# Optimization experiments

Hardware: AMD Instinct MI355X
Metric: run time of the kernel (lower is better)

Reference implementation:

```python
import jax, jax.numpy as jnp
import numpy as np

K_LAYERS = 2   # top-k layers kept in zeta routing
K_EXPERTS = 2  # top-k experts kept in alpha routing


def _topk_sparse_softmax(logits, k):
    """Keep top-k along last axis, set rest to -inf, softmax. logits [..., N]."""
    lead = logits.shape[:-1]
    n = logits.shape[-1]
    flat = logits.reshape(-1, n)
    vals, idx = jax.lax.top_k(flat, k)                      # [R,k]
    sparse = jnp.full_like(flat, -jnp.inf)
    rows = jnp.arange(flat.shape[0])[:, None]
    sparse = sparse.at[rows, idx].set(vals)
    return jax.nn.softmax(sparse, axis=-1).reshape(*lead, n)


def _lora_layer(h, W, b, A, B, zeta_l, alpha_l):
    """One backbone Linear + gated LoRA expert mixture + ReLU.
    h [B,in], W [out,in], A [E,r,in], B [E,out,r], zeta_l [B], alpha_l [B,E].
    """
    lin = h @ W.T + b                                       # [B,out]
    t = jnp.einsum('bi,eri->ber', h, A)                     # [B,E,r]
    tw = t * alpha_l[:, :, None]                            # weight experts early
    lora_sum = jnp.einsum('ber,eor->bo', tw, B)             # [B,out]
    return jax.nn.relu(lin + zeta_l[:, None] * lora_sum)


def _routing(domain_ids, dom_emb, layer_pos, Wi1, bi1, Wi2, bi2,
             Wa1, ba1, Wa2, ba2, gate_logits, R_benefit):
    M, H = dom_emb.shape
    L = layer_pos.shape[0]
    router_inp = jnp.concatenate([
        jnp.broadcast_to(dom_emb[:, None, :], (M, L, H)),
        jnp.broadcast_to(layer_pos[None, :, :], (M, L, H)),
    ], axis=-1)                                             # [M,L,2H]
    hz = jax.nn.relu(router_inp @ Wi1.T + bi1)
    zeta_logits = (hz @ Wi2.T + bi2)[..., 0]                # [M,L]
    zeta_all = _topk_sparse_softmax(zeta_logits, K_LAYERS)
    ha = jax.nn.relu(router_inp @ Wa1.T + ba1)
    alpha_logits = ha @ Wa2.T + ba2                         # [M,L,E]
    alpha_all = _topk_sparse_softmax(alpha_logits, K_EXPERTS)
    # gated benefit matrix, row-normalized
    R = jax.nn.softplus(gate_logits) * R_benefit
    R = R / jnp.clip(R.sum(-1, keepdims=True), 1e-12)
    zeta_agg = R @ zeta_all                                 # [M,L]
    alpha_agg = jnp.einsum('mn,nle->mle', R, alpha_all)     # [M,L,E]
    return zeta_agg[domain_ids], alpha_agg[domain_ids]      # [B,L],[B,L,E]


def setup_inputs() -> dict:
    key = jax.random.key(0)
    ks = jax.random.split(key, 32)
    Bsz, D0, D1, D2, D3 = 16384, 2048, 2048, 1024, 512
    E, r, M, H, L = 4, 8, 8, 64, 3
    s = 0.02
    return {
        'x': jax.random.normal(ks[0], (Bsz, D0), jnp.float32),
        'domain_ids': jax.random.randint(ks[1], (Bsz,), 0, M),
        'W1': jax.random.normal(ks[2], (D1, D0)) * s, 'b1': jnp.zeros((D1,)),
        'W2': jax.random.normal(ks[3], (D2, D1)) * s, 'b2': jnp.zeros((D2,)),
        'W3': jax.random.normal(ks[4], (D3, D2)) * s, 'b3': jnp.zeros((D3,)),
        'A1': jax.random.normal(ks[5], (E, r, D0)) * s, 'B1': jax.random.normal(ks[6], (E, D1, r)) * s,
        'A2': jax.random.normal(ks[7], (E, r, D1)) * s, 'B2': jax.random.normal(ks[8], (E, D2, r)) * s,
        'A3': jax.random.normal(ks[9], (E, r, D2)) * s, 'B3': jax.random.normal(ks[10], (E, D3, r)) * s,
        'dom_emb': jax.random.normal(ks[11], (M, H)) * s,
        'layer_pos': jax.random.normal(ks[12], (L, H)) * s,
        'Wi1': jax.random.normal(ks[13], (H, 2 * H)) * 0.1, 'bi1': jnp.zeros((H,)),
        'Wi2': jax.random.normal(ks[14], (1, H)) * 0.1, 'bi2': jnp.zeros((1,)),
        'Wa1': jax.random.normal(ks[15], (H, 2 * H)) * 0.1, 'ba1': jnp.zeros((H,)),
        'Wa2': jax.random.normal(ks[16], (E, H)) * 0.1, 'ba2': jnp.zeros((E,)),
        'gate_logits': jax.random.normal(ks[17], (M, M)) * 0.1,
        'R_benefit': jax.random.uniform(ks[18], (M, M)),
    }


def reference(x, domain_ids, W1, b1, W2, b2, W3, b3,
              A1, B1, A2, B2, A3, B3,
              dom_emb, layer_pos, Wi1, bi1, Wi2, bi2,
              Wa1, ba1, Wa2, ba2, gate_logits, R_benefit):
    zeta, alpha = _routing(domain_ids, dom_emb, layer_pos, Wi1, bi1, Wi2, bi2,
                           Wa1, ba1, Wa2, ba2, gate_logits, R_benefit)
    h = _lora_layer(x, W1, b1, A1, B1, zeta[:, 0], alpha[:, 0])
    h = _lora_layer(h, W2, b2, A2, B2, zeta[:, 1], alpha[:, 1])
    h = _lora_layer(h, W3, b3, A3, B3, zeta[:, 2], alpha[:, 2])
    return h
```

## Files before the change

### kernel.cpp

```cpp
#include <hip/hip_runtime.h>

typedef __bf16 bf16_t;
typedef __bf16 bf16x8 __attribute__((ext_vector_type(8)));
typedef __bf16 bf16x4_v __attribute__((ext_vector_type(4)));
typedef float f32x4 __attribute__((ext_vector_type(4)));

#define AS1 __attribute__((address_space(1)))
#define AS3 __attribute__((address_space(3)))

__device__ __forceinline__ void gload_lds16(const void* g, void* l) {
    __builtin_amdgcn_global_load_lds((AS1 void*)(void*)g, (AS3 void*)l, 16, 0, 0);
}

__global__ void routing_kernel(
    const float* __restrict__ dom_emb, const float* __restrict__ layer_pos,
    const float* __restrict__ Wi1, const float* __restrict__ bi1,
    const float* __restrict__ Wi2, const float* __restrict__ bi2,
    const float* __restrict__ Wa1, const float* __restrict__ ba1,
    const float* __restrict__ Wa2, const float* __restrict__ ba2,
    const float* __restrict__ gate_logits, const float* __restrict__ R_benefit,
    float* __restrict__ salpha)
{
    constexpr int M = 8, L = 3, E = 4, H = 64;
    __shared__ float zl[M * L];
    __shared__ float al[M * L][E];
    __shared__ float zeta_all[M][L];
    __shared__ float alpha_all[M][L][E];
    const int t = threadIdx.x;
    const int ml = t >> 3, js = t & 7;
    if (ml < M * L) {
        const int m = ml / L, l = ml % L;
        float zacc = 0.f;
        float aacc[E] = {0.f, 0.f, 0.f, 0.f};
        for (int jj = 0; jj < 8; ++jj) {
            const int j = js * 8 + jj;
            float hz = bi1[j], ha = ba1[j];
            for (int i = 0; i < H; ++i) {
                const float de = dom_emb[m * H + i];
                const float lp = layer_pos[l * H + i];
                hz += de * Wi1[j * 2 * H + i] + lp * Wi1[j * 2 * H + H + i];
                ha += de * Wa1[j * 2 * H + i] + lp * Wa1[j * 2 * H + H + i];
            }
            hz = fmaxf(hz, 0.f); ha = fmaxf(ha, 0.f);
            zacc += hz * Wi2[j];
            for (int e = 0; e < E; ++e) aacc[e] += ha * Wa2[e * H + j];
        }
        #pragma unroll
        for (int off = 4; off >= 1; off >>= 1) {
            zacc += __shfl_down(zacc, off, 8);
            for (int e = 0; e < E; ++e) aacc[e] += __shfl_down(aacc[e], off, 8);
        }
        if (js == 0) {
            zl[ml] = zacc + bi2[0];
            for (int e = 0; e < E; ++e) al[ml][e] = aacc[e] + ba2[e];
        }
    }
    __syncthreads();
    if (t < M) {
        const int m = t;
        float v[3] = { zl[m * L + 0], zl[m * L + 1], zl[m * L + 2] };
        int di = 0; float dv = v[0];
        for (int i = 1; i < 3; ++i) if (v[i] <= dv) { dv = v[i]; di = i; }
        float mx = -1e30f;
        for (int i = 0; i < 3; ++i) if (i != di) mx = fmaxf(mx, v[i]);
        float s = 0.f, ev[3];
        for (int i = 0; i < 3; ++i) { ev[i] = (i == di) ? 0.f : expf(v[i] - mx); s += ev[i]; }
        for (int i = 0; i < 3; ++i) zeta_all[m][i] = ev[i] / s;
        for (int l = 0; l < L; ++l) {
            float a[4];
            for (int e = 0; e < 4; ++e) a[e] = al[m * L + l][e];
            int i1 = 0;
            for (int e = 1; e < 4; ++e) if (a[e] > a[i1]) i1 = e;
            int i2 = -1;
            for (int e = 0; e < 4; ++e) { if (e == i1) continue; if (i2 < 0 || a[e] > a[i2]) i2 = e; }
            const float mx2 = fmaxf(a[i1], a[i2]);
            const float e1 = expf(a[i1] - mx2), e2 = expf(a[i2] - mx2);
            const float ss = e1 + e2;
            for (int e = 0; e < 4; ++e) alpha_all[m][l][e] = 0.f;
            alpha_all[m][l][i1] = e1 / ss;
            alpha_all[m][l][i2] = e2 / ss;
        }
    }
    __syncthreads();
    if (t < M) {
        const int m = t;
        float Rrow[8]; float rs = 0.f;
        for (int n = 0; n < M; ++n) {
            const float g = gate_logits[m * M + n];
            const float rr = log1pf(expf(g)) * R_benefit[m * M + n];
            Rrow[n] = rr; rs += rr;
        }
        rs = fmaxf(rs, 1e-12f);
        for (int l = 0; l < L; ++l) {
            float zag = 0.f, aag[4] = {0.f, 0.f, 0.f, 0.f};
            for (int n = 0; n < M; ++n) {
                const float w = Rrow[n] / rs;
                zag += w * zeta_all[n][l];
                for (int e = 0; e < 4; ++e) aag[e] += w * alpha_all[n][l][e];
            }
            for (int e = 0; e < 4; ++e) salpha[(m * L + l) * 4 + e] = zag * aag[e];
        }
    }
}

__global__ void cvt_fused(const float* __restrict__ s0, const float* __restrict__ s1,
                          const float* __restrict__ s2, const float* __restrict__ s3,
                          const float* __restrict__ s4, const float* __restrict__ s5,
                          bf16_t* __restrict__ dst)
{
    const int i = blockIdx.x * 256 + threadIdx.x;
    constexpr int b0 = 1048576;
    constexpr int b1 = b0 + 524288;
    constexpr int b2 = b1 + 131072;
    constexpr int b3 = b2 + 16384;
    constexpr int b4 = b3 + 16384;
    constexpr int b5 = b4 + 8192;
    if (i >= b5) return;
    const float* src; int rel;
    if (i < b0)      { src = s0; rel = i; }
    else if (i < b1) { src = s1; rel = i - b0; }
    else if (i < b2) { src = s2; rel = i - b1; }
    else if (i < b3) { src = s3; rel = i - b2; }
    else if (i < b4) { src = s4; rel = i - b3; }
    else             { src = s5; rel = i - b4; }
    const float4 v = ((const float4*)src)[rel];
    bf16x4_v o;
    o[0] = (__bf16)v.x; o[1] = (__bf16)v.y; o[2] = (__bf16)v.z; o[3] = (__bf16)v.w;
    ((bf16x4_v*)dst)[i] = o;
}

__global__ void bepi_fused(const float* __restrict__ B1, const float* __restrict__ B2,
                           const float* __restrict__ B3, bf16_t* __restrict__ dst)
{
    const int idx = blockIdx.x * 256 + threadIdx.x;
    constexpr int c1 = 2048 * 32, c2 = c1 + 1024 * 32, c3 = c2 + 512 * 32;
    if (idx >= c3) return;
    const float* B; int rel, Dout;
    if (idx < c1)      { B = B1; rel = idx;      Dout = 2048; }
    else if (idx < c2) { B = B2; rel = idx - c1; Dout = 1024; }
    else               { B = B3; rel = idx - c2; Dout = 512; }
    const int o = rel >> 5, c = rel & 31, e = c >> 3, r = c & 7;
    dst[idx] = (__bf16)B[((size_t)e * Dout + o) * 8 + r];
}

template<bool F32IN>
__global__ void __launch_bounds__(256) tw_kernel(
    const void* __restrict__ hin, bf16_t* __restrict__ xb_out,
    const bf16_t* __restrict__ Acat, const float* __restrict__ salpha,
    const int* __restrict__ dom, const int layer, const int K,
    bf16_t* __restrict__ TWb)
{
    const int t = threadIdx.x, wid = t >> 6, lane = t & 63;
    const int rb = blockIdx.x * 64 + wid * 16;
    const int ln15 = lane & 15, kg = (lane >> 4) * 8;
    const int row = rb + ln15;
    const int Kh = K >> 1;
    f32x4 a0l = {0.f,0.f,0.f,0.f}, a1l = {0.f,0.f,0.f,0.f};
    f32x4 a0h = {0.f,0.f,0.f,0.f}, a1h = {0.f,0.f,0.f,0.f};
    const bf16_t* pa0 = Acat + (size_t)ln15 * K + kg;
    const bf16_t* pa1 = pa0 + (size_t)16 * K;
    for (int k0 = 0; k0 < Kh; k0 += 32) {
        bf16x8 al, ah;
        if constexpr (F32IN) {
            const float* px = (const float*)hin + (size_t)row * K + k0 + kg;
            const float4 x0 = *(const float4*)px;
            const float4 x1 = *(const float4*)(px + 4);
            const float4 y0 = *(const float4*)(px + Kh);
            const float4 y1 = *(const float4*)(px + Kh + 4);
            al[0] = (__bf16)x0.x; al[1] = (__bf16)x0.y; al[2] = (__bf16)x0.z; al[3] = (__bf16)x0.w;
            al[4] = (__bf16)x1.x; al[5] = (__bf16)x1.y; al[6] = (__bf16)x1.z; al[7] = (__bf16)x1.w;
            ah[0] = (__bf16)y0.x; ah[1] = (__bf16)y0.y; ah[2] = (__bf16)y0.z; ah[3] = (__bf16)y0.w;
            ah[4] = (__bf16)y1.x; ah[5] = (__bf16)y1.y; ah[6] = (__bf16)y1.z; ah[7] = (__bf16)y1.w;
            *(bf16x8*)(xb_out + (size_t)row * K + k0 + kg) = al;
            *(bf16x8*)(xb_out + (size_t)row * K + Kh + k0 + kg) = ah;
        } else {
            al = *(const bf16x8*)((const bf16_t*)hin + (size_t)row * K + k0 + kg);
            ah = *(const bf16x8*)((const bf16_t*)hin + (size_t)row * K + Kh + k0 + kg);
        }
        const bf16x8 b0l = *(const bf16x8*)(pa0 + k0);
        const bf16x8 b1l = *(const bf16x8*)(pa1 + k0);
        const bf16x8 b0h = *(const bf16x8*)(pa0 + Kh + k0);
        const bf16x8 b1h = *(const bf16x8*)(pa1 + Kh + k0);
        a0l = __builtin_amdgcn_mfma_f32_16x16x32_bf16(al, b0l, a0l, 0, 0, 0);
        a1l = __builtin_amdgcn_mfma_f32_16x16x32_bf16(al, b1l, a1l, 0, 0, 0);
        a0h = __builtin_amdgcn_mfma_f32_16x16x32_bf16(ah, b0h, a0h, 0, 0, 0);
        a1h = __builtin_amdgcn_mfma_f32_16x16x32_bf16(ah, b1h, a1h, 0, 0, 0);
    }
    const f32x4 acc0 = a0l + a0h;
    const f32x4 acc1 = a1l + a1h;
    const int rbase = rb + (lane >> 4) * 4;
    #pragma unroll
    for (int i = 0; i < 4; ++i) {
        const int r2 = rbase + i;
        const int d = dom[r2];
        const float* sa = salpha + (d * 3 + layer) * 4;
        const float s0 = sa[ln15 >> 3];
        const float s1 = sa[2 + (ln15 >> 3)];
        TWb[(size_t)r2 * 32 + ln15]      = (__bf16)(acc0[i] * s0);
        TWb[(size_t)r2 * 32 + 16 + ln15] = (__bf16)(acc1[i] * s1);
    }
}


__device__ __forceinline__ void stage_chunk32(const bf16_t* g, char* chunk, int t) {
    const int row = t >> 2;
    const int sl = t & 3;
    const int src = sl ^ (((row >> 3) & 1) << 1);
    gload_lds16(g + (size_t)row * 32 + src * 8, chunk + t * 16);
}

template<int K>
__global__ void __launch_bounds__(512, 2) gemm_lora8(
    const bf16_t* __restrict__ Abuf, const bf16_t* __restrict__ Wbuf,
    const float* __restrict__ bias, const bf16_t* __restrict__ TWb,
    const bf16_t* __restrict__ Bepi, bf16_t* __restrict__ outp,
    const int N, const int nwg_n)
{
    __shared__ __align__(1024) char lds[131072];
    const int t = threadIdx.x;
    const int wid = t >> 6, lane = t & 63;
    const int wm = wid >> 2, wn = wid & 3, wnh = wn >> 1;
    const int cpx = gridDim.x >> 3;
    const int wg = (blockIdx.x & 7) * cpx + (blockIdx.x >> 3);
    const int row0 = (wg / nwg_n) * 256, col0 = (wg % nwg_n) * 256;

    const int r15 = lane & 15;
    const int swb = ((lane >> 4) ^ (((lane >> 3) & 1) << 1)) << 4;

    const char* aBase = lds + (wm << 14) + (r15 << 6) + swb;
    const char* bBase = lds + 65536 + (wnh << 14) + ((wn & 1) << 12) + (r15 << 6) + swb;
    char* const dBase = lds + t * 16;

    const int srow = t >> 2, ssl = t & 3;
    const int ssrc = ssl ^ (((srow >> 3) & 1) << 1);
    const bf16_t* sA = Abuf + (size_t)(row0 + srow) * K + ssrc * 8;
    const bf16_t* sB = Wbuf + (size_t)(col0 + srow) * K + ssrc * 8;
    constexpr size_t halfA = (size_t)128 * K;

    f32x4 acc[8][4] = {};
    bf16x8 aF[4], bF[4];

    #define RD_A(P, KQ, MB) do { _Pragma("unroll") for (int i_ = 0; i_ < 4; ++i_) \
        aF[i_] = *(const bf16x8*)(aBase + (P)*32768 + (KQ)*8192 + ((MB)+i_)*1024); } while (0)
    #define RD_B(P, KQ) do { _Pragma("unroll") for (int n_ = 0; n_ < 4; ++n_) \
        bF[n_] = *(const bf16x8*)(bBase + (P)*32768 + (KQ)*8192 + n_*1024); } while (0)

    auto mfma16 = [&](int mbase) {
        __builtin_amdgcn_s_setprio(1);
        #pragma unroll
        for (int mf = 0; mf < 4; ++mf)
            #pragma unroll
            for (int nf = 0; nf < 4; ++nf)
                acc[mbase + mf][nf] =
                    __builtin_amdgcn_mfma_f32_16x16x32_bf16(aF[mf], bF[nf], acc[mbase + mf][nf], 0, 0, 0);
        __builtin_amdgcn_s_setprio(0);
    };
    #define BAR() __builtin_amdgcn_s_barrier()

    constexpr int NT = K >> 6;

    gload_lds16(sA,              dBase + 0);
    gload_lds16(sA + halfA,      dBase + 16384);
    gload_lds16(sB,              dBase + 65536);
    gload_lds16(sB + halfA,      dBase + 65536 + 16384);
    gload_lds16(sA + 32,         dBase + 8192);
    gload_lds16(sA + halfA + 32, dBase + 24576);
    gload_lds16(sB + 32,         dBase + 65536 + 8192);
    gload_lds16(sB + halfA + 32, dBase + 65536 + 24576);
    asm volatile("s_waitcnt vmcnt(4)" ::: "memory");
    __builtin_amdgcn_s_barrier();

    const bf16_t* pA0 = sA + 64;
    const bf16_t* pA1 = sA + halfA + 64;
    const bf16_t* pB0 = sB + 64;
    const bf16_t* pB1 = sB + halfA + 64;

    #define TILE(P, MORE, TOFF) do {                                            \
                                           \
        RD_A(P, 0, 0);                                                           \
        RD_B(P, 0);                                                              \
        if (MORE) { gload_lds16(pA0 + (TOFF), dBase + ((P)^1)*32768 + 0);        \
                    gload_lds16(pA1 + (TOFF), dBase + ((P)^1)*32768 + 16384); }  \
        BAR();                                                                   \
        mfma16(0);                                                               \
                  \
        RD_A(P, 0, 4);                                                           \
        if (MORE) {                                                              \
            gload_lds16(pB0 + (TOFF), dBase + 65536 + ((P)^1)*32768 + 0);        \
            gload_lds16(pB1 + (TOFF), dBase + 65536 + ((P)^1)*32768 + 16384);    \
            asm volatile("s_waitcnt vmcnt(4)" ::: "memory");                     \
        } else {                                                                 \
            asm volatile("s_waitcnt vmcnt(0)" ::: "memory");                     \
        }                                                                        \
        BAR();                                                                   \
        mfma16(4);                                                               \
                                           \
        RD_A(P, 1, 4);                                                           \
        RD_B(P, 1);                                                              \
        if (MORE) { gload_lds16(pA0 + (TOFF) + 32, dBase + ((P)^1)*32768 + 8192);  \
                    gload_lds16(pA1 + (TOFF) + 32, dBase + ((P)^1)*32768 + 24576);} \
        BAR();                                                                   \
        mfma16(4);                                                               \
                \
        RD_A(P, 1, 0);                                                           \
        if (MORE) {                                                              \
            gload_lds16(pB0 + (TOFF) + 32, dBase + 65536 + ((P)^1)*32768 + 8192);  \
            gload_lds16(pB1 + (TOFF) + 32, dBase + 65536 + ((P)^1)*32768 + 24576); \
            asm volatile("s_waitcnt vmcnt(4)" ::: "memory");                     \
        }                                                                        \
        BAR();                                                                   \
        mfma16(0);                                                               \
    } while (0)

    #pragma unroll 1
    for (int T = 0; T < NT - 2; T += 2) {
        TILE(0, true, 0);
        TILE(1, true, 64);
        pA0 += 128; pA1 += 128; pB0 += 128; pB1 += 128;
    }
    TILE(0, true, 0);
    TILE(1, false, 64);

    {
        __builtin_amdgcn_s_barrier();
        stage_chunk32(TWb + (size_t)row0 * 32,          lds + 0,             t);
        stage_chunk32(TWb + (size_t)(row0 + 128) * 32,  lds + 16384,         t);
        stage_chunk32(Bepi + (size_t)col0 * 32,         lds + 65536,         t);
        stage_chunk32(Bepi + (size_t)(col0 + 128) * 32, lds + 65536 + 16384, t);
        asm volatile("s_waitcnt vmcnt(0)" ::: "memory");
        __builtin_amdgcn_s_barrier();
        RD_B(0, 0);
        RD_A(0, 0, 0);
        mfma16(0);
        RD_A(0, 0, 4);
        mfma16(4);
    }

    const int orow = row0 + wm * 128 + (lane >> 4) * 4;
    const int ocol = col0 + wn * 64 + r15;
    #pragma unroll
    for (int nf = 0; nf < 4; ++nf) {
        const int col = ocol + nf * 16;
        const float bn = bias[col];
        #pragma unroll
        for (int mf = 0; mf < 8; ++mf) {
            const int rbase = orow + mf * 16;
            #pragma unroll
            for (int i = 0; i < 4; ++i) {
                const float v = fmaxf(acc[mf][nf][i] + bn, 0.f);
                outp[(size_t)(rbase + i) * N + col] = (__bf16)v;
            }
        }
    }
    #undef TILE
    #undef RD_A
    #undef RD_B
    #undef BAR
}

#define BM 128
#define BN 128
#define BK 32

template<bool OUT_F32, int K>
__global__ void __launch_bounds__(256) gemm_lora(
    const bf16_t* __restrict__ Abuf, const bf16_t* __restrict__ Wbuf,
    const float* __restrict__ bias, const bf16_t* __restrict__ TWb,
    const bf16_t* __restrict__ Bepi, void* __restrict__ outp,
    const int N)
{
    __shared__ bf16_t lA[BM * BK];
    __shared__ bf16_t lB[BN * BK];
    const int t = threadIdx.x;
    const int row0 = blockIdx.y * BM;
    const int col0 = blockIdx.x * BN;
    const int wid = t >> 6, lane = t & 63;
    const int wr = wid >> 1, wc = wid & 1;
    const int ln15 = lane & 15, kg = (lane >> 4) * 8;
    const int srow = t >> 2, sg8 = (t & 3) * 8;
    const bf16_t* gA = Abuf + (size_t)(row0 + srow) * K + sg8;
    const bf16_t* gB = Wbuf + (size_t)(col0 + srow) * K + sg8;
    bf16_t* ldA  = &lA[t * 8];
    bf16_t* ldA2 = &lA[2048 + t * 8];
    bf16_t* ldB  = &lB[t * 8];
    bf16_t* ldB2 = &lB[2048 + t * 8];
    f32x4 acc[4][4] = {};
    const int aoff = (wr * 64 + ln15) * BK + kg;
    const int boff = (wc * 64 + ln15) * BK + kg;

    auto compute_tile = [&]() {
        bf16x8 af[4], bfr[4];
        #pragma unroll
        for (int m = 0; m < 4; ++m) af[m] = *(const bf16x8*)&lA[aoff + m * 16 * BK];
        #pragma unroll
        for (int n = 0; n < 4; ++n) bfr[n] = *(const bf16x8*)&lB[boff + n * 16 * BK];
        #pragma unroll
        for (int m = 0; m < 4; ++m)
            #pragma unroll
            for (int n = 0; n < 4; ++n)
                acc[m][n] = __builtin_amdgcn_mfma_f32_16x16x32_bf16(af[m], bfr[n], acc[m][n], 0, 0, 0);
    };

    constexpr size_t half = (size_t)64 * K;
    constexpr int nk = K / BK;
    #pragma unroll 1
    for (int kt = 0; kt < nk; ++kt) {
        gload_lds16(gA + kt * BK, ldA);
        gload_lds16(gA + half + kt * BK, ldA2);
        gload_lds16(gB + kt * BK, ldB);
        gload_lds16(gB + half + kt * BK, ldB2);
        __syncthreads();
        compute_tile();
        __syncthreads();
    }
    gload_lds16(TWb + (size_t)(row0 + srow) * 32 + sg8, ldA);
    gload_lds16(TWb + (size_t)(row0 + 64 + srow) * 32 + sg8, ldA2);
    gload_lds16(Bepi + (size_t)(col0 + srow) * 32 + sg8, ldB);
    gload_lds16(Bepi + (size_t)(col0 + 64 + srow) * 32 + sg8, ldB2);
    __syncthreads();
    compute_tile();

    const int orow = row0 + wr * 64 + (lane >> 4) * 4;
    const int ocol = col0 + wc * 64 + ln15;
    #pragma unroll
    for (int n = 0; n < 4; ++n) {
        const int col = ocol + n * 16;
        const float bn = bias[col];
        #pragma unroll
        for (int m = 0; m < 4; ++m) {
            const int rbase = orow + m * 16;
            #pragma unroll
            for (int i = 0; i < 4; ++i) {
                const float v = fmaxf(acc[m][n][i] + bn, 0.f);
                if constexpr (OUT_F32)
                    ((float*)outp)[(size_t)(rbase + i) * N + col] = v;
                else
                    ((bf16_t*)outp)[(size_t)(rbase + i) * N + col] = (__bf16)v;
            }
        }
    }
}

extern "C" void kernel_launch(void* const* d_in, const int* in_sizes, int n_in,
                              void* d_out, int out_size, void* d_ws, size_t ws_size,
                              hipStream_t stream)
{
    const float* x    = (const float*)d_in[0];
    const int*   dom  = (const int*)d_in[1];
    const float* W1   = (const float*)d_in[2];  const float* b1  = (const float*)d_in[3];
    const float* W2   = (const float*)d_in[4];  const float* b2  = (const float*)d_in[5];
    const float* W3   = (const float*)d_in[6];  const float* b3  = (const float*)d_in[7];
    const float* A1   = (const float*)d_in[8];  const float* B1  = (const float*)d_in[9];
    const float* A2   = (const float*)d_in[10]; const float* B2  = (const float*)d_in[11];
    const float* A3   = (const float*)d_in[12]; const float* B3  = (const float*)d_in[13];
    const float* dome = (const float*)d_in[14]; const float* lpos = (const float*)d_in[15];
    const float* Wi1  = (const float*)d_in[16]; const float* bi1 = (const float*)d_in[17];
    const float* Wi2  = (const float*)d_in[18]; const float* bi2 = (const float*)d_in[19];
    const float* Wa1  = (const float*)d_in[20]; const float* ba1 = (const float*)d_in[21];
    const float* Wa2  = (const float*)d_in[22]; const float* ba2 = (const float*)d_in[23];
    const float* gate = (const float*)d_in[24]; const float* Rb  = (const float*)d_in[25];
    (void)in_sizes; (void)n_in; (void)out_size; (void)ws_size;

    constexpr int Bsz = 16384, D0 = 2048, D1 = 2048, D2 = 1024, D3 = 512;

    char* ws = (char*)d_ws;
    size_t off = 0;
    auto alloc = [&](size_t bytes) -> void* {
        void* p = ws + off;
        off = (off + bytes + 255) & ~(size_t)255;
        return p;
    };
    float*  salpha = (float*) alloc(8 * 3 * 4 * sizeof(float));
    bf16_t* W1b = (bf16_t*)alloc((size_t)D1 * D0 * 2);
    bf16_t* W2b = (bf16_t*)alloc((size_t)D2 * D1 * 2);
    bf16_t* W3b = (bf16_t*)alloc((size_t)D3 * D2 * 2);
    bf16_t* Ac1 = (bf16_t*)alloc((size_t)32 * D0 * 2);
    bf16_t* Ac2 = (bf16_t*)alloc((size_t)32 * D1 * 2);
    bf16_t* Ac3 = (bf16_t*)alloc((size_t)32 * D2 * 2);
    bf16_t* Be1 = (bf16_t*)alloc((size_t)D1 * 32 * 2);
    bf16_t* Be2 = (bf16_t*)alloc((size_t)D2 * 32 * 2);
    bf16_t* Be3 = (bf16_t*)alloc((size_t)D3 * 32 * 2);
    bf16_t* TWb = (bf16_t*)alloc((size_t)Bsz * 32 * 2);
    bf16_t* xb  = (bf16_t*)alloc((size_t)Bsz * D0 * 2);
    bf16_t* h1b = (bf16_t*)alloc((size_t)Bsz * D1 * 2);
    bf16_t* h2b = xb;

    routing_kernel<<<1, 256, 0, stream>>>(dome, lpos, Wi1, bi1, Wi2, bi2,
                                          Wa1, ba1, Wa2, ba2, gate, Rb, salpha);

    cvt_fused<<<6816, 256, 0, stream>>>(W1, W2, W3, A1, A2, A3, W1b);
    bepi_fused<<<448, 256, 0, stream>>>(B1, B2, B3, Be1);

    tw_kernel<true><<<Bsz / 64, 256, 0, stream>>>(x, xb, Ac1, salpha, dom, 0, D0, TWb);
    gemm_lora8<2048><<<(Bsz / 256) * (D1 / 256), 512, 0, stream>>>(xb, W1b, b1, TWb, Be1, h1b, D1, D1 / 256);
    tw_kernel<false><<<Bsz / 64, 256, 0, stream>>>(h1b, nullptr, Ac2, salpha, dom, 1, D1, TWb);
    gemm_lora8<2048><<<(Bsz / 256) * (D2 / 256), 512, 0, stream>>>(h1b, W2b, b2, TWb, Be2, h2b, D2, D2 / 256);
    tw_kernel<false><<<Bsz / 64, 256, 0, stream>>>(h2b, nullptr, Ac3, salpha, dom, 2, D2, TWb);
    gemm_lora<true, 1024><<<dim3(D3 / BN, Bsz / BM), 256, 0, stream>>>(h2b, W3b, b3, TWb, Be3, d_out, D3);
}
```

Baseline: 393.0 us.

## Merge prep kernels into one launch and stage GEMM epilogue through LDS

Routing, weight conversion and B-epilogue repacking now run as one kernel launch distinguished by block index, replacing three launches. The gemm_lora8 epilogue writes bias+ReLU results into a swizzled per-wave LDS buffer and reads them back as 16-byte vectors. This replaces scattered 2-byte global stores with coalesced row stores. The cost is extra LDS traffic and a barrier, and the single routing block now runs alongside the conversion blocks.

```diff
diff --git a/kernel.cpp b/kernel.cpp
--- a/kernel.cpp
+++ b/kernel.cpp
@@ -12,135 +12,131 @@
     __builtin_amdgcn_global_load_lds((AS1 void*)(void*)g, (AS3 void*)l, 16, 0, 0);
 }
 
-__global__ void routing_kernel(
+__global__ void __launch_bounds__(256) prep_kernel(
     const float* __restrict__ dom_emb, const float* __restrict__ layer_pos,
     const float* __restrict__ Wi1, const float* __restrict__ bi1,
     const float* __restrict__ Wi2, const float* __restrict__ bi2,
     const float* __restrict__ Wa1, const float* __restrict__ ba1,
     const float* __restrict__ Wa2, const float* __restrict__ ba2,
     const float* __restrict__ gate_logits, const float* __restrict__ R_benefit,
-    float* __restrict__ salpha)
+    float* __restrict__ salpha,
+    const float* __restrict__ s0, const float* __restrict__ s1,
+    const float* __restrict__ s2, const float* __restrict__ s3,
+    const float* __restrict__ s4, const float* __restrict__ s5,
+    bf16_t* __restrict__ wdst,
+    const float* __restrict__ B1, const float* __restrict__ B2,
+    const float* __restrict__ B3, bf16_t* __restrict__ bedst)
 {
-    constexpr int M = 8, L = 3, E = 4, H = 64;
-    __shared__ float zl[M * L];
-    __shared__ float al[M * L][E];
-    __shared__ float zeta_all[M][L];
-    __shared__ float alpha_all[M][L][E];
+    const int blk = blockIdx.x;
     const int t = threadIdx.x;
-    const int ml = t >> 3, js = t & 7;
-    if (ml < M * L) {
-        const int m = ml / L, l = ml % L;
-        float zacc = 0.f;
-        float aacc[E] = {0.f, 0.f, 0.f, 0.f};
-        for (int jj = 0; jj < 8; ++jj) {
-            const int j = js * 8 + jj;
-            float hz = bi1[j], ha = ba1[j];
-            for (int i = 0; i < H; ++i) {
-                const float de = dom_emb[m * H + i];
-                const float lp = layer_pos[l * H + i];
-                hz += de * Wi1[j * 2 * H + i] + lp * Wi1[j * 2 * H + H + i];
-                ha += de * Wa1[j * 2 * H + i] + lp * Wa1[j * 2 * H + H + i];
-            }
-            hz = fmaxf(hz, 0.f); ha = fmaxf(ha, 0.f);
-            zacc += hz * Wi2[j];
-            for (int e = 0; e < E; ++e) aacc[e] += ha * Wa2[e * H + j];
+    if (blk == 0) {
+        constexpr int M = 8, L = 3, E = 4, H = 64;
+        __shared__ float zl[M * L];
+        __shared__ float al[M * L][E];
+        __shared__ float zeta_all[M][L];
+        __shared__ float alpha_all[M][L][E];
+        const int ml = t >> 3, js = t & 7;
+        if (ml < M * L) {
+            const int m = ml / L, l = ml % L;
+            float zacc = 0.f;
+            float aacc[E] = {0.f, 0.f, 0.f, 0.f};
+            for (int jj = 0; jj < 8; ++jj) {
+                const int j = js * 8 + jj;
+                float hz = bi1[j], ha = ba1[j];
+                for (int i = 0; i < H; ++i) {
+                    const float de = dom_emb[m * H + i];
+                    const float lp = layer_pos[l * H + i];
+                    hz += de * Wi1[j * 2 * H + i] + lp * Wi1[j * 2 * H + H + i];
+                    ha += de * Wa1[j * 2 * H + i] + lp * Wa1[j * 2 * H + H + i];
+                }
+                hz = fmaxf(hz, 0.f); ha = fmaxf(ha, 0.f);
+                zacc += hz * Wi2[j];
+                for (int e = 0; e < E; ++e) aacc[e] += ha * Wa2[e * H + j];
+            }
+            #pragma unroll
+            for (int off = 4; off >= 1; off >>= 1) {
+                zacc += __shfl_down(zacc, off, 8);
+                for (int e = 0; e < E; ++e) aacc[e] += __shfl_down(aacc[e], off, 8);
+            }
+            if (js == 0) {
+                zl[ml] = zacc + bi2[0];
+                for (int e = 0; e < E; ++e) al[ml][e] = aacc[e] + ba2[e];
+            }
         }
-        #pragma unroll
-        for (int off = 4; off >= 1; off >>= 1) {
-            zacc += __shfl_down(zacc, off, 8);
-            for (int e = 0; e < E; ++e) aacc[e] += __shfl_down(aacc[e], off, 8);
+        __syncthreads();
+        if (t < M) {
+            const int m = t;
+            float v[3] = { zl[m * L + 0], zl[m * L + 1], zl[m * L + 2] };
+            int di = 0; float dv = v[0];
+            for (int i = 1; i < 3; ++i) if (v[i] <= dv) { dv = v[i]; di = i; }
+            float mx = -1e30f;
+            for (int i = 0; i < 3; ++i) if (i != di) mx = fmaxf(mx, v[i]);
+            float s = 0.f, ev[3];
+            for (int i = 0; i < 3; ++i) { ev[i] = (i == di) ? 0.f : expf(v[i] - mx); s += ev[i]; }
+            for (int i = 0; i < 3; ++i) zeta_all[m][i] = ev[i] / s;
+            for (int l = 0; l < L; ++l) {
+                float a[4];
+                for (int e = 0; e < 4; ++e) a[e] = al[m * L + l][e];
+                int i1 = 0;
+                for (int e = 1; e < 4; ++e) if (a[e] > a[i1]) i1 = e;
+                int i2 = -1;
+                for (int e = 0; e < 4; ++e) { if (e == i1) continue; if (i2 < 0 || a[e] > a[i2]) i2 = e; }
+                const float mx2 = fmaxf(a[i1], a[i2]);
+                const float e1 = expf(a[i1] - mx2), e2 = expf(a[i2] - mx2);
+                const float ss = e1 + e2;
+                for (int e = 0; e < 4; ++e) alpha_all[m][l][e] = 0.f;
+                alpha_all[m][l][i1] = e1 / ss;
+                alpha_all[m][l][i2] = e2 / ss;
+            }
         }
-        if (js == 0) {
-            zl[ml] = zacc + bi2[0];
-            for (int e = 0; e < E; ++e) al[ml][e] = aacc[e] + ba2[e];
+        __syncthreads();
+        if (t < M) {
+            const int m = t;
+            float Rrow[8]; float rs = 0.f;
+            for (int n = 0; n < M; ++n) {
+                const float g = gate_logits[m * M + n];
+                const float rr = log1pf(expf(g)) * R_benefit[m * M + n];
+                Rrow[n] = rr; rs += rr;
+            }
+            rs = fmaxf(rs, 1e-12f);
+            for (int l = 0; l < L; ++l) {
+                float zag = 0.f, aag[4] = {0.f, 0.f, 0.f, 0.f};
+                for (int n = 0; n < M; ++n) {
+                    const float w = Rrow[n] / rs;
+                    zag += w * zeta_all[n][l];
+                    for (int e = 0; e < 4; ++e) aag[e] += w * alpha_all[n][l][e];
+                }
+                for (int e = 0; e < 4; ++e) salpha[(m * L + l) * 4 + e] = zag * aag[e];
+            }
         }
-    }
-    __syncthreads();
-    if (t < M) {
-        const int m = t;
-        float v[3] = { zl[m * L + 0], zl[m * L + 1], zl[m * L + 2] };
-        int di = 0; float dv = v[0];
-        for (int i = 1; i < 3; ++i) if (v[i] <= dv) { dv = v[i]; di = i; }
-        float mx = -1e30f;
-        for (int i = 0; i < 3; ++i) if (i != di) mx = fmaxf(mx, v[i]);
-        float s = 0.f, ev[3];
-        for (int i = 0; i < 3; ++i) { ev[i] = (i == di) ? 0.f : expf(v[i] - mx); s += ev[i]; }
-        for (int i = 0; i < 3; ++i) zeta_all[m][i] = ev[i] / s;
-        for (int l = 0; l < L; ++l) {
-            float a[4];
-            for (int e = 0; e < 4; ++e) a[e] = al[m * L + l][e];
-            int i1 = 0;
-            for (int e = 1; e < 4; ++e) if (a[e] > a[i1]) i1 = e;
-            int i2 = -1;
-            for (int e = 0; e < 4; ++e) { if (e == i1) continue; if (i2 < 0 || a[e] > a[i2]) i2 = e; }
-            const float mx2 = fmaxf(a[i1], a[i2]);
-            const float e1 = expf(a[i1] - mx2), e2 = expf(a[i2] - mx2);
-            const float ss = e1 + e2;
-            for (int e = 0; e < 4; ++e) alpha_all[m][l][e] = 0.f;
-            alpha_all[m][l][i1] = e1 / ss;
-            alpha_all[m][l][i2] = e2 / ss;
-        }
-    }
-    __syncthreads();
-    if (t < M) {
-        const int m = t;
-        float Rrow[8]; float rs = 0.f;
-        for (int n = 0; n < M; ++n) {
-            const float g = gate_logits[m * M + n];
-            const float rr = log1pf(expf(g)) * R_benefit[m * M + n];
-            Rrow[n] = rr; rs += rr;
-        }
-        rs = fmaxf(rs, 1e-12f);
-        for (int l = 0; l < L; ++l) {
-            float zag = 0.f, aag[4] = {0.f, 0.f, 0.f, 0.f};
-            for (int n = 0; n < M; ++n) {
-                const float w = Rrow[n] / rs;
-                zag += w * zeta_all[n][l];
-                for (int e = 0; e < 4; ++e) aag[e] += w * alpha_all[n][l][e];
-            }
-            for (int e = 0; e < 4; ++e) salpha[(m * L + l) * 4 + e] = zag * aag[e];
-        }
-    }
-}
-
-__global__ void cvt_fused(const float* __restrict__ s0, const float* __restrict__ s1,
-                          const float* __restrict__ s2, const float* __restrict__ s3,
-                          const float* __restrict__ s4, const float* __restrict__ s5,
-                          bf16_t* __restrict__ dst)
-{
-    const int i = blockIdx.x * 256 + threadIdx.x;
-    constexpr int b0 = 1048576;
-    constexpr int b1 = b0 + 524288;
-    constexpr int b2 = b1 + 131072;
-    constexpr int b3 = b2 + 16384;
-    constexpr int b4 = b3 + 16384;
-    constexpr int b5 = b4 + 8192;
-    if (i >= b5) return;
-    const float* src; int rel;
-    if (i < b0)      { src = s0; rel = i; }
-    else if (i < b1) { src = s1; rel = i - b0; }
-    else if (i < b2) { src = s2; rel = i - b1; }
-    else if (i < b3) { src = s3; rel = i - b2; }
-    else if (i < b4) { src = s4; rel = i - b3; }
-    else             { src = s5; rel = i - b4; }
-    const float4 v = ((const float4*)src)[rel];
-    bf16x4_v o;
-    o[0] = (__bf16)v.x; o[1] = (__bf16)v.y; o[2] = (__bf16)v.z; o[3] = (__bf16)v.w;
-    ((bf16x4_v*)dst)[i] = o;
-}
-
-__global__ void bepi_fused(const float* __restrict__ B1, const float* __restrict__ B2,
-                           const float* __restrict__ B3, bf16_t* __restrict__ dst)
-{
-    const int idx = blockIdx.x * 256 + threadIdx.x;
-    constexpr int c1 = 2048 * 32, c2 = c1 + 1024 * 32, c3 = c2 + 512 * 32;
-    if (idx >= c3) return;
-    const float* B; int rel, Dout;
-    if (idx < c1)      { B = B1; rel = idx;      Dout = 2048; }
-    else if (idx < c2) { B = B2; rel = idx - c1; Dout = 1024; }
-    else               { B = B3; rel = idx - c2; Dout = 512; }
-    const int o = rel >> 5, c = rel & 31, e = c >> 3, r = c & 7;
-    dst[idx] = (__bf16)B[((size_t)e * Dout + o) * 8 + r];
+    } else if (blk <= 6816) {
+        const int i = (blk - 1) * 256 + t;
+        constexpr int b0 = 1048576;
+        constexpr int b1 = b0 + 524288;
+        constexpr int b2 = b1 + 131072;
+        constexpr int b3 = b2 + 16384;
+        constexpr int b4 = b3 + 16384;
+        const float* src; int rel;
+        if (i < b0)      { src = s0; rel = i; }
+        else if (i < b1) { src = s1; rel = i - b0; }
+        else if (i < b2) { src = s2; rel = i - b1; }
+        else if (i < b3) { src = s3; rel = i - b2; }
+        else if (i < b4) { src = s4; rel = i - b3; }
+        else             { src = s5; rel = i - b4; }
+        const float4 v = ((const float4*)src)[rel];
+        bf16x4_v o;
+        o[0] = (__bf16)v.x; o[1] = (__bf16)v.y; o[2] = (__bf16)v.z; o[3] = (__bf16)v.w;
+        ((bf16x4_v*)wdst)[i] = o;
+    } else {
+        const int idx = (blk - 6817) * 256 + t;
+        constexpr int c1 = 2048 * 32, c2 = c1 + 1024 * 32;
+        const float* B; int rel, Dout;
+        if (idx < c1)      { B = B1; rel = idx;      Dout = 2048; }
+        else if (idx < c2) { B = B2; rel = idx - c1; Dout = 1024; }
+        else               { B = B3; rel = idx - c2; Dout = 512; }
+        const int o = rel >> 5, c = rel & 31, e = c >> 3, r = c & 7;
+        bedst[idx] = (__bf16)B[((size_t)e * Dout + o) * 8 + r];
+    }
 }
 
 template<bool F32IN>
@@ -276,14 +272,12 @@
     const bf16_t* pB1 = sB + halfA + 64;
 
     #define TILE(P, MORE, TOFF) do {                                            \
-                                           \
         RD_A(P, 0, 0);                                                           \
         RD_B(P, 0);                                                              \
         if (MORE) { gload_lds16(pA0 + (TOFF), dBase + ((P)^1)*32768 + 0);        \
                     gload_lds16(pA1 + (TOFF), dBase + ((P)^1)*32768 + 16384); }  \
         BAR();                                                                   \
         mfma16(0);                                                               \
-                  \
         RD_A(P, 0, 4);                                                           \
         if (MORE) {                                                              \
             gload_lds16(pB0 + (TOFF), dBase + 65536 + ((P)^1)*32768 + 0);        \
@@ -294,14 +288,12 @@
         }                                                                        \
         BAR();                                                                   \
         mfma16(4);                                                               \
-                                           \
         RD_A(P, 1, 4);                                                           \
         RD_B(P, 1);                                                              \
         if (MORE) { gload_lds16(pA0 + (TOFF) + 32, dBase + ((P)^1)*32768 + 8192);  \
                     gload_lds16(pA1 + (TOFF) + 32, dBase + ((P)^1)*32768 + 24576);} \
         BAR();                                                                   \
         mfma16(4);                                                               \
-                \
         RD_A(P, 1, 0);                                                           \
         if (MORE) {                                                              \
             gload_lds16(pB0 + (TOFF) + 32, dBase + 65536 + ((P)^1)*32768 + 8192);  \
@@ -336,20 +328,40 @@
         mfma16(4);
     }
 
-    const int orow = row0 + wm * 128 + (lane >> 4) * 4;
-    const int ocol = col0 + wn * 64 + r15;
-    #pragma unroll
-    for (int nf = 0; nf < 4; ++nf) {
-        const int col = ocol + nf * 16;
-        const float bn = bias[col];
+    __builtin_amdgcn_s_barrier();
+    {
+        char* eb = lds + wid * 2048;
+        const int rloc = (lane >> 4) * 4;
+        const int g = lane >> 4;
+        const int orow0 = row0 + wm * 128;
+        const int ocol0 = col0 + wn * 64;
+        float bcol[4];
+        #pragma unroll
+        for (int nf = 0; nf < 4; ++nf) bcol[nf] = bias[ocol0 + nf * 16 + r15];
+        const int rdrow = lane >> 3;
+        const int rdcolb = (lane & 7) * 16;
+        const int rdoff0 = rdrow * 128 + (rdcolb ^ ((rdrow >> 2) << 5));
+        const int rdoff1 = (rdrow + 8) * 128 + (rdcolb ^ (((rdrow + 8) >> 2) << 5));
+        bf16_t* outbase = outp + (size_t)ocol0 + (lane & 7) * 8;
         #pragma unroll
         for (int mf = 0; mf < 8; ++mf) {
-            const int rbase = orow + mf * 16;
             #pragma unroll
             for (int i = 0; i < 4; ++i) {
-                const float v = fmaxf(acc[mf][nf][i] + bn, 0.f);
-                outp[(size_t)(rbase + i) * N + col] = (__bf16)v;
-            }
+                const int r = rloc + i;
+                #pragma unroll
+                for (int nf = 0; nf < 4; ++nf) {
+                    const float v = fmaxf(acc[mf][nf][i] + bcol[nf], 0.f);
+                    *(bf16_t*)(eb + r * 128 + ((nf ^ g) * 32 + r15 * 2)) = (__bf16)v;
+                }
+            }
+            __builtin_amdgcn_sched_barrier(0);
+            asm volatile("" ::: "memory");
+            const bf16x8 v0 = *(const bf16x8*)(eb + rdoff0);
+            const bf16x8 v1 = *(const bf16x8*)(eb + rdoff1);
+            asm volatile("" ::: "memory");
+            __builtin_amdgcn_sched_barrier(0);
+            *(bf16x8*)(outbase + (size_t)(orow0 + mf * 16 + rdrow) * N) = v0;
+            *(bf16x8*)(outbase + (size_t)(orow0 + mf * 16 + 8 + rdrow) * N) = v1;
         }
     }
     #undef TILE
@@ -485,11 +497,10 @@
     bf16_t* h1b = (bf16_t*)alloc((size_t)Bsz * D1 * 2);
     bf16_t* h2b = xb;
 
-    routing_kernel<<<1, 256, 0, stream>>>(dome, lpos, Wi1, bi1, Wi2, bi2,
-                                          Wa1, ba1, Wa2, ba2, gate, Rb, salpha);
-
-    cvt_fused<<<6816, 256, 0, stream>>>(W1, W2, W3, A1, A2, A3, W1b);
-    bepi_fused<<<448, 256, 0, stream>>>(B1, B2, B3, Be1);
+    prep_kernel<<<7265, 256, 0, stream>>>(
+        dome, lpos, Wi1, bi1, Wi2, bi2, Wa1, ba1, Wa2, ba2, gate, Rb, salpha,
+        W1, W2, W3, A1, A2, A3, W1b,
+        B1, B2, B3, Be1);
 
     tw_kernel<true><<<Bsz / 64, 256, 0, stream>>>(x, xb, Ac1, salpha, dom, 0, D0, TWb);
     gemm_lora8<2048><<<(Bsz / 256) * (D1 / 256), 512, 0, stream>>>(xb, W1b, b1, TWb, Be1, h1b, D1, D1 / 256);
```

Result: faster. 370.0 us (-5.8%).
